# Kernel tuning notes

Measured on AMD Instinct MI355X. Metric: run time of the kernel, lower is better.

Reference implementation:

```python
import jax, jax.numpy as jnp
import numpy as np

N, C, S = 262144, 256, 16
BN_EPS = 1e-5


def setup_inputs() -> dict:
    key = jax.random.key(0)
    ks = jax.random.split(key, 8)
    x = jax.random.normal(ks[0], (N, C), dtype=jnp.float32)
    # strictly increasing cumulative offsets ending at N (guarantees nonzero counts)
    rng = np.random.default_rng(0)
    cuts = np.sort(rng.choice(np.arange(1, N), size=S - 1, replace=False))
    o = jnp.asarray(np.concatenate([cuts, [N]]), dtype=jnp.int64)
    # linear2_: Linear(C, C) (+ReLU, no BN in this branch)
    W2 = jax.random.normal(ks[1], (C, C), dtype=jnp.float32) / np.sqrt(C)
    b2 = jax.random.normal(ks[2], (C,), dtype=jnp.float32) * 0.01
    # linear1_: Linear(2C, C) + BatchNorm1d(C) + ReLU
    W1 = jax.random.normal(ks[3], (2 * C, C), dtype=jnp.float32) / np.sqrt(2 * C)
    b1 = jax.random.normal(ks[4], (C,), dtype=jnp.float32) * 0.01
    gamma = jnp.ones((C,), dtype=jnp.float32)
    beta = jnp.zeros((C,), dtype=jnp.float32)
    run_mean = jax.random.normal(ks[5], (C,), dtype=jnp.float32) * 0.01
    run_var = jnp.ones((C,), dtype=jnp.float32)
    return {"x": x, "o": o, "W2": W2, "b2": b2, "W1": W1, "b1": b1,
            "gamma": gamma, "beta": beta, "run_mean": run_mean, "run_var": run_var}


def reference(x, o, W2, b2, W1, b1, gamma, beta, run_mean, run_var):
    n, c = x.shape
    num_seg = o.shape[0]
    # segment id of each point: first offset strictly greater than index
    seg_ids = jnp.searchsorted(o, jnp.arange(n), side="right")  # [N]
    counts = jnp.diff(o, prepend=0).astype(x.dtype)             # [S]
    sums = jax.ops.segment_sum(x, seg_ids, num_segments=num_seg)  # [S, C]
    means = sums / counts[:, None]
    # linear2_ on per-segment mean, broadcast back to points
    h = jax.nn.relu(means @ W2 + b2)                            # [S, C]
    xc = jnp.concatenate([x, h[seg_ids]], axis=1)               # [N, 2C]
    # linear1_: Linear + BatchNorm1d (inference, running stats) + ReLU
    y = xc @ W1 + b1
    y = (y - run_mean) * jax.lax.rsqrt(run_var + BN_EPS) * gamma + beta
    return jax.nn.relu(y)
```

## Files before the change

### kernel.cpp

```cpp
#include <hip/hip_runtime.h>

#define N_PTS 262144
#define C_DIM 256
#define S_SEG 16

typedef __attribute__((ext_vector_type(8))) short bf16x8;
typedef __attribute__((ext_vector_type(4))) float f32x4;

__device__ __forceinline__ short f2bf(float f) {
    unsigned u = __builtin_bit_cast(unsigned, f);
    u += 0x7FFF + ((u >> 16) & 1);
    return (short)(u >> 16);
}

__global__ void k0_norm_o(const int* __restrict__ o_raw, int* __restrict__ o32) {
    int t = threadIdx.x;
    if (t < S_SEG) {
        bool is64 = (o_raw[1] == 0);
        o32[t] = is64 ? o_raw[2 * t] : o_raw[t];
    }
}

__global__ __launch_bounds__(256) void k1_segsum(const float* __restrict__ x,
                                                 const int* __restrict__ o32,
                                                 float* __restrict__ sums) {
    __shared__ int o_s[S_SEG];
    __shared__ float4 partv[256];
    __shared__ int pseg[256];
    int t = threadIdx.x;
    if (t < S_SEG) o_s[t] = o32[t];
    __syncthreads();

    int rsub = t >> 6, cg = t & 63;
    int row0 = blockIdx.x * 256 + rsub * 64;
    const float4* xv = (const float4*)x;

    int cur = 0;
#pragma unroll
    for (int j = 0; j < S_SEG; ++j) cur += (row0 >= o_s[j]);
    int next = o_s[cur];

    float4 acc = make_float4(0.f, 0.f, 0.f, 0.f);
    for (int i = 0; i < 64; ++i) {
        int row = row0 + i;
        if (row >= next) {
            atomicAdd(&sums[cur * C_DIM + cg * 4 + 0], acc.x);
            atomicAdd(&sums[cur * C_DIM + cg * 4 + 1], acc.y);
            atomicAdd(&sums[cur * C_DIM + cg * 4 + 2], acc.z);
            atomicAdd(&sums[cur * C_DIM + cg * 4 + 3], acc.w);
            acc = make_float4(0.f, 0.f, 0.f, 0.f);
            do { cur++; next = o_s[cur]; } while (row >= next);
        }
        float4 v = xv[row * 64 + cg];
        acc.x += v.x; acc.y += v.y; acc.z += v.z; acc.w += v.w;
    }
    partv[t] = acc;
    pseg[t] = cur;
    __syncthreads();

    if (t < 64) {
        float4 a = partv[t];
        int s = pseg[t];
        for (int i = 1; i < 4; ++i) {
            int idx = i * 64 + t;
            int s2 = pseg[idx];
            float4 a2 = partv[idx];
            if (s2 == s) {
                a.x += a2.x; a.y += a2.y; a.z += a2.z; a.w += a2.w;
            } else {
                atomicAdd(&sums[s * C_DIM + t * 4 + 0], a.x);
                atomicAdd(&sums[s * C_DIM + t * 4 + 1], a.y);
                atomicAdd(&sums[s * C_DIM + t * 4 + 2], a.z);
                atomicAdd(&sums[s * C_DIM + t * 4 + 3], a.w);
                s = s2; a = a2;
            }
        }
        atomicAdd(&sums[s * C_DIM + t * 4 + 0], a.x);
        atomicAdd(&sums[s * C_DIM + t * 4 + 1], a.y);
        atomicAdd(&sums[s * C_DIM + t * 4 + 2], a.z);
        atomicAdd(&sums[s * C_DIM + t * 4 + 3], a.w);
    }
}

__global__ __launch_bounds__(256) void k2_small(const float* __restrict__ sums,
                                                const int* __restrict__ o32,
                                                const float* __restrict__ W2,
                                                const float* __restrict__ b2,
                                                const float* __restrict__ W1,
                                                const float* __restrict__ b1,
                                                const float* __restrict__ gamma,
                                                const float* __restrict__ beta,
                                                const float* __restrict__ rmean,
                                                const float* __restrict__ rvar,
                                                float* __restrict__ Cseg,
                                                short* __restrict__ W1s) {
    int t = threadIdx.x;
    int blk = blockIdx.x;
    if (blk < S_SEG) {
        __shared__ float mean_s[C_DIM];
        __shared__ float h_s[C_DIM];
        int s = blk;
        int lo = (s == 0) ? 0 : o32[s - 1];
        float inv = 1.0f / (float)(o32[s] - lo);
        mean_s[t] = sums[s * C_DIM + t] * inv;
        __syncthreads();
        float acc = b2[t];
#pragma unroll 4
        for (int k = 0; k < C_DIM; ++k) acc = fmaf(mean_s[k], W2[k * C_DIM + t], acc);
        h_s[t] = fmaxf(acc, 0.0f);
        __syncthreads();
        float acc2 = 0.f;
#pragma unroll 4
        for (int k = 0; k < C_DIM; ++k) acc2 = fmaf(h_s[k], W1[(C_DIM + k) * C_DIM + t], acc2);
        float sc = gamma[t] * rsqrtf(rvar[t] + 1e-5f);
        Cseg[s * C_DIM + t] = (b1[t] + acc2 - rmean[t]) * sc + beta[t];
    } else {
        int base = (blk - S_SEG) * 8192;
        for (int i = 0; i < 32; ++i) {
            int idx = base + i * 256 + t;
            int k = idx >> 8, c = idx & 255;
            float sc = gamma[c] * rsqrtf(rvar[c] + 1e-5f);
            float v = W1[k * C_DIM + c] * sc;
            int kb2 = k >> 5, q = (k >> 3) & 3, j = k & 7, nsub = c >> 4, r = c & 15;
            int off = ((kb2 * 16 + nsub) * 64 + q * 16 + r) * 8 + j;
            W1s[off] = f2bf(v);
        }
    }
}

__global__ __launch_bounds__(256) void k3_gemm(const float* __restrict__ x,
                                               const short* __restrict__ W1s,
                                               const float* __restrict__ Cseg,
                                               const int* __restrict__ o32,
                                               float* __restrict__ out) {
    __shared__ __align__(16) short As[4 * 2 * 64 * 8];
    __shared__ float Cs[S_SEG * C_DIM];
    __shared__ int o_s[S_SEG];

    int t = threadIdx.x;
    int wave = t >> 6, lane = t & 63;
    int q = lane >> 4, r = lane & 15;
    int wc = wave;
    int m0 = blockIdx.x * 64;

    if (t < S_SEG) o_s[t] = o32[t];
    for (int i = t; i < S_SEG * C_DIM; i += 256) Cs[i] = Cseg[i];

    f32x4 acc[4][4];
#pragma unroll
    for (int mt = 0; mt < 4; ++mt)
#pragma unroll
        for (int nt = 0; nt < 4; ++nt)
            acc[mt][nt] = (f32x4){0.f, 0.f, 0.f, 0.f};

    const float4* xv = (const float4*)x;
    int arow = t >> 3;
    int akc = t & 7;
    int kt_w = akc >> 2, q_w = akc & 3;

    for (int kb = 0; kb < 4; ++kb) {
        long g0 = (long)(m0 + arow) * 64 + kb * 16 + akc * 2;
        long g1 = (long)(m0 + 32 + arow) * 64 + kb * 16 + akc * 2;
        float4 c00 = xv[g0], c01 = xv[g0 + 1];
        float4 c10 = xv[g1], c11 = xv[g1 + 1];

        __syncthreads();

        {
            int mt0 = arow >> 4, r0 = arow & 15;
            int slot0 = (mt0 * 2 + kt_w) * 64 + q_w * 16 + (r0 ^ q_w);
            bf16x8 w0;
            w0[0] = f2bf(c00.x); w0[1] = f2bf(c00.y); w0[2] = f2bf(c00.z); w0[3] = f2bf(c00.w);
            w0[4] = f2bf(c01.x); w0[5] = f2bf(c01.y); w0[6] = f2bf(c01.z); w0[7] = f2bf(c01.w);
            *(bf16x8*)&As[slot0 * 8] = w0;

            int row1 = 32 + arow;
            int mt1 = row1 >> 4, r1 = row1 & 15;
            int slot1 = (mt1 * 2 + kt_w) * 64 + q_w * 16 + (r1 ^ q_w);
            bf16x8 w1;
            w1[0] = f2bf(c10.x); w1[1] = f2bf(c10.y); w1[2] = f2bf(c10.z); w1[3] = f2bf(c10.w);
            w1[4] = f2bf(c11.x); w1[5] = f2bf(c11.y); w1[6] = f2bf(c11.z); w1[7] = f2bf(c11.w);
            *(bf16x8*)&As[slot1 * 8] = w1;
        }
        __syncthreads();

#pragma unroll
        for (int kt = 0; kt < 2; ++kt) {
            bf16x8 a[4], b[4];
#pragma unroll
            for (int mt = 0; mt < 4; ++mt)
                a[mt] = *(const bf16x8*)&As[((mt * 2 + kt) * 64 + q * 16 + (r ^ q)) * 8];
#pragma unroll
            for (int nt = 0; nt < 4; ++nt) {
                int nsub = wc * 4 + nt;
                b[nt] = *(const bf16x8*)&W1s[(((kb * 2 + kt) * 16 + nsub) * 64 + lane) * 8];
            }
#pragma unroll
            for (int mt = 0; mt < 4; ++mt)
#pragma unroll
                for (int nt = 0; nt < 4; ++nt)
                    acc[mt][nt] = __builtin_amdgcn_mfma_f32_16x16x32_bf16(a[mt], b[nt], acc[mt][nt], 0, 0, 0);
        }
    }

#pragma unroll
    for (int mt = 0; mt < 4; ++mt) {
#pragma unroll
        for (int i = 0; i < 4; ++i) {
            int row = m0 + mt * 16 + q * 4 + i;
            int s = 0;
#pragma unroll
            for (int j = 0; j < S_SEG; ++j) s += (row >= o_s[j]);
#pragma unroll
            for (int nt = 0; nt < 4; ++nt) {
                int col = wc * 64 + nt * 16 + r;
                float v = acc[mt][nt][i] + Cs[s * C_DIM + col];
                out[(long)row * C_DIM + col] = fmaxf(v, 0.0f);
            }
        }
    }
}

extern "C" void kernel_launch(void* const* d_in, const int* in_sizes, int n_in,
                              void* d_out, int out_size, void* d_ws, size_t ws_size,
                              hipStream_t stream) {
    const float* x     = (const float*)d_in[0];
    const int*   o     = (const int*)d_in[1];
    const float* W2    = (const float*)d_in[2];
    const float* b2    = (const float*)d_in[3];
    const float* W1    = (const float*)d_in[4];
    const float* b1    = (const float*)d_in[5];
    const float* gamma = (const float*)d_in[6];
    const float* beta  = (const float*)d_in[7];
    const float* rmean = (const float*)d_in[8];
    const float* rvar  = (const float*)d_in[9];
    float* out = (float*)d_out;

    float* sums = (float*)d_ws;
    float* Cseg = (float*)((char*)d_ws + 16384);
    int*   o32  = (int*)((char*)d_ws + 32768);
    short* W1s  = (short*)((char*)d_ws + 65536);

    hipMemsetAsync(d_ws, 0, 16384, stream);
    k0_norm_o<<<1, 64, 0, stream>>>(o, o32);
    k1_segsum<<<1024, 256, 0, stream>>>(x, o32, sums);
    k2_small<<<24, 256, 0, stream>>>(sums, o32, W2, b2, W1, b1, gamma, beta, rmean, rvar, Cseg, W1s);
    k3_gemm<<<4096, 256, 0, stream>>>(x, W1s, Cseg, o32, out);
}
```

Measured before the change: 608.1 us.

## Double-buffer GEMM A tile, drop offset kernel, reverse block order, nontemporal stores

Removes the separate offset-normalisation kernel, so each kernel reads the raw offsets directly. In the GEMM, the A-tile LDS buffer is double-buffered so the next x slice is loaded and converted while MFMAs run on the current one, with one barrier per k-step instead of two. Blocks are processed in reverse order, likely so the GEMM first reads the x rows the segment-sum kernel touched last and may still be cached. The epilogue reads Cseg from global memory instead of staging it in LDS, and writes the output with nontemporal stores. These changes cut launch overhead, LDS use and stalls, at the cost of slightly more global traffic in the epilogue.

```diff
diff --git a/kernel.cpp b/kernel.cpp
--- a/kernel.cpp
+++ b/kernel.cpp
@@ -1,6 +1,5 @@
 #include <hip/hip_runtime.h>
 
-#define N_PTS 262144
 #define C_DIM 256
 #define S_SEG 16
 
@@ -13,22 +12,18 @@
     return (short)(u >> 16);
 }
 
-__global__ void k0_norm_o(const int* __restrict__ o_raw, int* __restrict__ o32) {
-    int t = threadIdx.x;
-    if (t < S_SEG) {
-        bool is64 = (o_raw[1] == 0);
-        o32[t] = is64 ? o_raw[2 * t] : o_raw[t];
-    }
+__device__ __forceinline__ int o_get(const int* __restrict__ o_raw, int i) {
+    return (o_raw[1] == 0) ? o_raw[2 * i] : o_raw[i];
 }
 
 __global__ __launch_bounds__(256) void k1_segsum(const float* __restrict__ x,
-                                                 const int* __restrict__ o32,
+                                                 const int* __restrict__ o_raw,
                                                  float* __restrict__ sums) {
     __shared__ int o_s[S_SEG];
     __shared__ float4 partv[256];
     __shared__ int pseg[256];
     int t = threadIdx.x;
-    if (t < S_SEG) o_s[t] = o32[t];
+    if (t < S_SEG) o_s[t] = o_get(o_raw, t);
     __syncthreads();
 
     int rsub = t >> 6, cg = t & 63;
@@ -83,7 +78,7 @@
 }
 
 __global__ __launch_bounds__(256) void k2_small(const float* __restrict__ sums,
-                                                const int* __restrict__ o32,
+                                                const int* __restrict__ o_raw,
                                                 const float* __restrict__ W2,
                                                 const float* __restrict__ b2,
                                                 const float* __restrict__ W1,
@@ -100,8 +95,8 @@
         __shared__ float mean_s[C_DIM];
         __shared__ float h_s[C_DIM];
         int s = blk;
-        int lo = (s == 0) ? 0 : o32[s - 1];
-        float inv = 1.0f / (float)(o32[s] - lo);
+        int lo = (s == 0) ? 0 : o_get(o_raw, s - 1);
+        float inv = 1.0f / (float)(o_get(o_raw, s) - lo);
         mean_s[t] = sums[s * C_DIM + t] * inv;
         __syncthreads();
         float acc = b2[t];
@@ -131,20 +126,18 @@
 __global__ __launch_bounds__(256) void k3_gemm(const float* __restrict__ x,
                                                const short* __restrict__ W1s,
                                                const float* __restrict__ Cseg,
-                                               const int* __restrict__ o32,
+                                               const int* __restrict__ o_raw,
                                                float* __restrict__ out) {
-    __shared__ __align__(16) short As[4 * 2 * 64 * 8];
-    __shared__ float Cs[S_SEG * C_DIM];
+    __shared__ __align__(16) short As[2][4 * 2 * 64 * 8];
     __shared__ int o_s[S_SEG];
 
     int t = threadIdx.x;
     int wave = t >> 6, lane = t & 63;
     int q = lane >> 4, r = lane & 15;
     int wc = wave;
-    int m0 = blockIdx.x * 64;
-
-    if (t < S_SEG) o_s[t] = o32[t];
-    for (int i = t; i < S_SEG * C_DIM; i += 256) Cs[i] = Cseg[i];
+    int m0 = (int)(gridDim.x - 1 - blockIdx.x) * 64;
+
+    if (t < S_SEG) o_s[t] = o_get(o_raw, t);
 
     f32x4 acc[4][4];
 #pragma unroll
@@ -157,49 +150,59 @@
     int arow = t >> 3;
     int akc = t & 7;
     int kt_w = akc >> 2, q_w = akc & 3;
+    int mt0 = arow >> 4, r0 = arow & 15;
+    int slot0 = (mt0 * 2 + kt_w) * 64 + q_w * 16 + (r0 ^ q_w);
+    int row1 = 32 + arow, mt1 = row1 >> 4, r1 = row1 & 15;
+    int slot1 = (mt1 * 2 + kt_w) * 64 + q_w * 16 + (r1 ^ q_w);
+    long gbase0 = (long)(m0 + arow) * 64 + akc * 2;
+    long gbase1 = (long)(m0 + 32 + arow) * 64 + akc * 2;
+
+    float4 c00, c01, c10, c11;
+    c00 = xv[gbase0]; c01 = xv[gbase0 + 1];
+    c10 = xv[gbase1]; c11 = xv[gbase1 + 1];
+    {
+        bf16x8 w0, w1;
+        w0[0] = f2bf(c00.x); w0[1] = f2bf(c00.y); w0[2] = f2bf(c00.z); w0[3] = f2bf(c00.w);
+        w0[4] = f2bf(c01.x); w0[5] = f2bf(c01.y); w0[6] = f2bf(c01.z); w0[7] = f2bf(c01.w);
+        *(bf16x8*)&As[0][slot0 * 8] = w0;
+        w1[0] = f2bf(c10.x); w1[1] = f2bf(c10.y); w1[2] = f2bf(c10.z); w1[3] = f2bf(c10.w);
+        w1[4] = f2bf(c11.x); w1[5] = f2bf(c11.y); w1[6] = f2bf(c11.z); w1[7] = f2bf(c11.w);
+        *(bf16x8*)&As[0][slot1 * 8] = w1;
+    }
+    __syncthreads();
 
     for (int kb = 0; kb < 4; ++kb) {
-        long g0 = (long)(m0 + arow) * 64 + kb * 16 + akc * 2;
-        long g1 = (long)(m0 + 32 + arow) * 64 + kb * 16 + akc * 2;
-        float4 c00 = xv[g0], c01 = xv[g0 + 1];
-        float4 c10 = xv[g1], c11 = xv[g1 + 1];
-
-        __syncthreads();
-
-        {
-            int mt0 = arow >> 4, r0 = arow & 15;
-            int slot0 = (mt0 * 2 + kt_w) * 64 + q_w * 16 + (r0 ^ q_w);
-            bf16x8 w0;
+        if (kb < 3) {
+            long o = (long)(kb + 1) * 16;
+            c00 = xv[gbase0 + o]; c01 = xv[gbase0 + o + 1];
+            c10 = xv[gbase1 + o]; c11 = xv[gbase1 + o + 1];
+        }
+        const short* Ab = As[kb & 1];
+#pragma unroll
+        for (int kt = 0; kt < 2; ++kt) {
+            bf16x8 a[4], b[4];
+#pragma unroll
+            for (int mt = 0; mt < 4; ++mt)
+                a[mt] = *(const bf16x8*)&Ab[((mt * 2 + kt) * 64 + q * 16 + (r ^ q)) * 8];
+#pragma unroll
+            for (int nt = 0; nt < 4; ++nt)
+                b[nt] = *(const bf16x8*)&W1s[(((kb * 2 + kt) * 16 + wc * 4 + nt) * 64 + lane) * 8];
+#pragma unroll
+            for (int mt = 0; mt < 4; ++mt)
+#pragma unroll
+                for (int nt = 0; nt < 4; ++nt)
+                    acc[mt][nt] = __builtin_amdgcn_mfma_f32_16x16x32_bf16(a[mt], b[nt], acc[mt][nt], 0, 0, 0);
+        }
+        if (kb < 3) {
+            short* Aw = As[(kb + 1) & 1];
+            bf16x8 w0, w1;
             w0[0] = f2bf(c00.x); w0[1] = f2bf(c00.y); w0[2] = f2bf(c00.z); w0[3] = f2bf(c00.w);
             w0[4] = f2bf(c01.x); w0[5] = f2bf(c01.y); w0[6] = f2bf(c01.z); w0[7] = f2bf(c01.w);
-            *(bf16x8*)&As[slot0 * 8] = w0;
-
-            int row1 = 32 + arow;
-            int mt1 = row1 >> 4, r1 = row1 & 15;
-            int slot1 = (mt1 * 2 + kt_w) * 64 + q_w * 16 + (r1 ^ q_w);
-            bf16x8 w1;
+            *(bf16x8*)&Aw[slot0 * 8] = w0;
             w1[0] = f2bf(c10.x); w1[1] = f2bf(c10.y); w1[2] = f2bf(c10.z); w1[3] = f2bf(c10.w);
             w1[4] = f2bf(c11.x); w1[5] = f2bf(c11.y); w1[6] = f2bf(c11.z); w1[7] = f2bf(c11.w);
-            *(bf16x8*)&As[slot1 * 8] = w1;
-        }
-        __syncthreads();
-
-#pragma unroll
-        for (int kt = 0; kt < 2; ++kt) {
-            bf16x8 a[4], b[4];
-#pragma unroll
-            for (int mt = 0; mt < 4; ++mt)
-                a[mt] = *(const bf16x8*)&As[((mt * 2 + kt) * 64 + q * 16 + (r ^ q)) * 8];
-#pragma unroll
-            for (int nt = 0; nt < 4; ++nt) {
-                int nsub = wc * 4 + nt;
-                b[nt] = *(const bf16x8*)&W1s[(((kb * 2 + kt) * 16 + nsub) * 64 + lane) * 8];
-            }
-#pragma unroll
-            for (int mt = 0; mt < 4; ++mt)
-#pragma unroll
-                for (int nt = 0; nt < 4; ++nt)
-                    acc[mt][nt] = __builtin_amdgcn_mfma_f32_16x16x32_bf16(a[mt], b[nt], acc[mt][nt], 0, 0, 0);
+            *(bf16x8*)&Aw[slot1 * 8] = w1;
+            __syncthreads();
         }
     }
 
@@ -214,8 +217,8 @@
 #pragma unroll
             for (int nt = 0; nt < 4; ++nt) {
                 int col = wc * 64 + nt * 16 + r;
-                float v = acc[mt][nt][i] + Cs[s * C_DIM + col];
-                out[(long)row * C_DIM + col] = fmaxf(v, 0.0f);
+                float v = acc[mt][nt][i] + Cseg[s * C_DIM + col];
+                __builtin_nontemporal_store(fmaxf(v, 0.0f), &out[(long)row * C_DIM + col]);
             }
         }
     }
@@ -238,12 +241,10 @@
 
     float* sums = (float*)d_ws;
     float* Cseg = (float*)((char*)d_ws + 16384);
-    int*   o32  = (int*)((char*)d_ws + 32768);
     short* W1s  = (short*)((char*)d_ws + 65536);
 
     hipMemsetAsync(d_ws, 0, 16384, stream);
-    k0_norm_o<<<1, 64, 0, stream>>>(o, o32);
-    k1_segsum<<<1024, 256, 0, stream>>>(x, o32, sums);
-    k2_small<<<24, 256, 0, stream>>>(sums, o32, W2, b2, W1, b1, gamma, beta, rmean, rvar, Cseg, W1s);
-    k3_gemm<<<4096, 256, 0, stream>>>(x, W1s, Cseg, o32, out);
-}
+    k1_segsum<<<1024, 256, 0, stream>>>(x, o, sums);
+    k2_small<<<24, 256, 0, stream>>>(sums, o, W2, b2, W1, b1, gamma, beta, rmean, rvar, Cseg, W1s);
+    k3_gemm<<<4096, 256, 0, stream>>>(x, W1s, Cseg, o, out);
+}
```

After: 600.9 us. Within noise of the previous version (-1.2%).
